# Optimization experiments

Hardware: AMD Instinct MI355X
Metric: run time of the kernel (lower is better)

Reference implementation:

```python
import jax, jax.numpy as jnp
import numpy as np

B, N, F, H, MH = 8, 1024, 768, 12, 3072
DH = F // H
EPS = 1e-5

def _ln(x, g, b):
    mu = jnp.mean(x, axis=-1, keepdims=True)
    var = jnp.mean(jnp.square(x - mu), axis=-1, keepdims=True)
    return (x - mu) * jax.lax.rsqrt(var + EPS) * g + b

def setup_inputs() -> dict:
    key = jax.random.key(0)
    ks = jax.random.split(key, 16)
    s = 1.0 / np.sqrt(F)
    sm = 1.0 / np.sqrt(MH)
    return {
        "x": jax.random.normal(ks[0], (B, N, F), dtype=jnp.float32),
        "Wq": jax.random.uniform(ks[1], (F, F), jnp.float32, -s, s),
        "bq": jax.random.uniform(ks[2], (F,), jnp.float32, -s, s),
        "Wk": jax.random.uniform(ks[3], (F, F), jnp.float32, -s, s),
        "bk": jax.random.uniform(ks[4], (F,), jnp.float32, -s, s),
        "Wv": jax.random.uniform(ks[5], (F, F), jnp.float32, -s, s),
        "bv": jax.random.uniform(ks[6], (F,), jnp.float32, -s, s),
        "Wo": jax.random.uniform(ks[7], (F, F), jnp.float32, -s, s),
        "bo": jax.random.uniform(ks[8], (F,), jnp.float32, -s, s),
        "ln1_g": jnp.ones((F,), jnp.float32),
        "ln1_b": jnp.zeros((F,), jnp.float32),
        "ln2_g": jnp.ones((F,), jnp.float32),
        "ln2_b": jnp.zeros((F,), jnp.float32),
        "W1": jax.random.uniform(ks[9], (F, MH), jnp.float32, -s, s),
        "b1": jax.random.uniform(ks[10], (MH,), jnp.float32, -s, s),
        "W2": jax.random.uniform(ks[11], (MH, F), jnp.float32, -sm, sm),
        "b2": jax.random.uniform(ks[12], (F,), jnp.float32, -sm, sm),
    }

def reference(x, Wq, bq, Wk, bk, Wv, bv, Wo, bo, ln1_g, ln1_b, ln2_g, ln2_b, W1, b1, W2, b2):
    xn = _ln(x, ln1_g, ln1_b)
    # low-rank (here full-rank, rank=-1) QKV projections, split into heads -> [b,h,n,dh]
    q = (xn @ Wq + bq).reshape(B, N, H, DH).transpose(0, 2, 1, 3)
    k = (xn @ Wk + bk).reshape(B, N, H, DH).transpose(0, 2, 1, 3)
    v = (xn @ Wv + bv).reshape(B, N, H, DH).transpose(0, 2, 1, 3)
    # note: original scales by sqrt(feats), NOT sqrt(d_head)
    score = jax.nn.softmax(jnp.einsum('bhif,bhjf->bhij', q, k) / jnp.sqrt(jnp.float32(F)), axis=-1)
    attn = jnp.einsum('bhij,bhjf->bhif', score, v)
    attn = attn.transpose(0, 2, 1, 3).reshape(B, N, F)
    out = (attn @ Wo + bo) + x  # dropout p=0.0
    h = _ln(out, ln2_g, ln2_b)
    h = jax.nn.gelu(h @ W1 + b1, approximate=False)
    h = jax.nn.gelu(h @ W2 + b2, approximate=False)  # second GELU per source
    return h + out
```

## Files before the change

kernel.cpp:

```cpp
#include <hip/hip_runtime.h>
#include <math.h>

#define B_ 8
#define N_ 1024
#define F_ 768
#define H_ 12
#define DH_ 64
#define MH_ 3072
#define MROWS (B_ * N_)

typedef unsigned short u16;
typedef unsigned int u32;
typedef __bf16 bf16x8 __attribute__((ext_vector_type(8)));
typedef float f32x4 __attribute__((ext_vector_type(4)));

__device__ inline f32x4 mfma16(bf16x8 a, bf16x8 b, f32x4 c) {
  return __builtin_amdgcn_mfma_f32_16x16x32_bf16(a, b, c, 0, 0, 0);
}

__device__ inline u16 f2bu(float f) {
  u32 b = __builtin_bit_cast(u32, f);
  b += 0x7fffu + ((b >> 16) & 1u);
  return (u16)(b >> 16);
}
__device__ inline float bu2f(u16 u) {
  u32 x = ((u32)u) << 16;
  return __builtin_bit_cast(float, x);
}
__device__ inline float gelu_f(float x) {
  float u = x * (0.7978845608028654f + 0.035677408136300125f * x * x);
  float t = exp2f(-2.8853900817779268f * fabsf(u));
  float th = (1.0f - t) / (1.0f + t);
  th = copysignf(th, u);
  return 0.5f * x * (1.0f + th);
}

#define AS1 __attribute__((address_space(1)))
#define AS3 __attribute__((address_space(3)))
__device__ inline void glds16(const void* g, void* l) {
  __builtin_amdgcn_global_load_lds((const AS1 void*)g, (AS3 void*)l, 16, 0, 0);
}

__global__ __launch_bounds__(256) void prep_weights(
    const float* __restrict__ Wq, const float* __restrict__ Wk,
    const float* __restrict__ Wv, const float* __restrict__ Wo,
    const float* __restrict__ W1, const float* __restrict__ W2,
    u16* __restrict__ Wqkvt, u16* __restrict__ Wot,
    u16* __restrict__ W1t, u16* __restrict__ W2t) {
  __shared__ float tile[64][65];
  int z = blockIdx.z;
  const float* in; u16* out; int R, C;
  if (z == 0)      { in = Wq; out = Wqkvt;                       R = 768;  C = 768; }
  else if (z == 1) { in = Wk; out = Wqkvt + 768 * 768;           R = 768;  C = 768; }
  else if (z == 2) { in = Wv; out = Wqkvt + 2 * 768 * 768;       R = 768;  C = 768; }
  else if (z == 3) { in = Wo; out = Wot;                         R = 768;  C = 768; }
  else if (z == 4) { in = W1; out = W1t;                         R = 768;  C = 3072; }
  else             { in = W2; out = W2t;                         R = 3072; C = 768; }
  int r0 = blockIdx.y << 6, c0 = blockIdx.x << 6;
  if (r0 >= R || c0 >= C) return;
  int t = threadIdx.x;
#pragma unroll
  for (int i = 0; i < 16; ++i) {
    int idx = t + (i << 8);
    int r = idx >> 6, c = idx & 63;
    tile[r][c] = in[(size_t)(r0 + r) * C + (c0 + c)];
  }
  __syncthreads();
#pragma unroll
  for (int i = 0; i < 16; ++i) {
    int idx = t + (i << 8);
    int rr = idx >> 6, cc = idx & 63;
    out[(size_t)(c0 + rr) * R + (r0 + cc)] = f2bu(tile[cc][rr]);
  }
}

__device__ inline float ldf(const float* p) { return *p; }
__device__ inline float ldf(const u16* p) { return bu2f(*p); }

template <typename Tin>
__global__ __launch_bounds__(256) void ln_to_bf16(
    const Tin* __restrict__ X, const float* __restrict__ gw,
    const float* __restrict__ bw, u16* __restrict__ Y) {
  int row = blockIdx.x;
  int t = threadIdx.x;
  const Tin* xr = X + (size_t)row * F_;
  float v0 = ldf(&xr[t]), v1 = ldf(&xr[t + 256]), v2 = ldf(&xr[t + 512]);
  float s = v0 + v1 + v2;
  float ss = v0 * v0 + v1 * v1 + v2 * v2;
#pragma unroll
  for (int off = 1; off < 64; off <<= 1) {
    s += __shfl_xor(s, off, 64);
    ss += __shfl_xor(ss, off, 64);
  }
  __shared__ float red[8];
  int wid = t >> 6, lane = t & 63;
  if (lane == 0) { red[wid] = s; red[4 + wid] = ss; }
  __syncthreads();
  s = red[0] + red[1] + red[2] + red[3];
  ss = red[4] + red[5] + red[6] + red[7];
  float mu = s * (1.0f / F_);
  float var = ss * (1.0f / F_) - mu * mu;
  float rstd = rsqrtf(var + 1e-5f);
  u16* yr = Y + (size_t)row * F_;
  yr[t] = f2bu((v0 - mu) * rstd * gw[t] + bw[t]);
  yr[t + 256] = f2bu((v1 - mu) * rstd * gw[t + 256] + bw[t + 256]);
  yr[t + 512] = f2bu((v2 - mu) * rstd * gw[t + 512] + bw[t + 512]);
}

template <int MODE>
__global__ __launch_bounds__(256, 2) void gemm_t(
    const u16* __restrict__ A, const u16* __restrict__ Bt,
    const float* __restrict__ b0, const float* __restrict__ b1,
    const float* __restrict__ b2, void* __restrict__ outp,
    const void* __restrict__ resid, int Ndim, int Kdim, float qscale) {
  __shared__ __attribute__((aligned(16))) u16 As[2][2][128][32];
  __shared__ __attribute__((aligned(16))) u16 Bs[2][2][128][32];
  int t = threadIdx.x;
  int lane = t & 63, wid = t >> 6;

  int nwg = gridDim.x;
  int q8 = nwg >> 3;
  int bid = blockIdx.x;
  int swz = (bid & 7) * q8 + (bid >> 3);
  int nnt = Ndim >> 7;
  int mt = swz / nnt, nt = swz - mt * nnt;
  int row0 = mt << 7, col0 = nt << 7;

  int wr = (wid >> 1) << 6;
  int wc = (wid & 1) << 6;
  int lr = lane & 15, lk = (lane >> 4) << 3;
  int rbase = (lane >> 4) << 2;
  f32x4 zero = {0.f, 0.f, 0.f, 0.f};
  f32x4 acc[4][4];
#pragma unroll
  for (int m = 0; m < 4; ++m)
#pragma unroll
    for (int n = 0; n < 4; ++n) acc[m][n] = zero;

  int srow = (wid << 5) + (lane >> 2);
  int scol = (lane & 3) << 3;
  const u16* Ag = A + (size_t)(row0 + srow) * Kdim + scol;
  const u16* Bg = Bt + (size_t)(col0 + srow) * Kdim + scol;
  char* AsB = (char*)&As[0][0][0][0] + (wid << 11);
  char* BsB = (char*)&Bs[0][0][0][0] + (wid << 11);

  auto STAGE = [&](int buf, int kt) {
    int ab = buf << 14;
#pragma unroll
    for (int kh = 0; kh < 2; ++kh) {
#pragma unroll
      for (int i = 0; i < 2; ++i) {
        glds16(Ag + (size_t)(i << 4) * Kdim + kt + (kh << 5),
               AsB + ab + (kh << 13) + (i << 10));
        glds16(Bg + (size_t)(i << 4) * Kdim + kt + (kh << 5),
               BsB + ab + (kh << 13) + (i << 10));
      }
    }
  };

  int nk = Kdim >> 6;
  STAGE(0, 0);
  if (nk > 1) STAGE(1, 64);

  for (int ki = 0; ki < nk; ++ki) {
    int buf = ki & 1;
    if (ki + 1 < nk) {
      asm volatile("s_waitcnt vmcnt(8)" ::: "memory");
    } else {
      asm volatile("s_waitcnt vmcnt(0)" ::: "memory");
    }
    __builtin_amdgcn_sched_barrier(0);
    __builtin_amdgcn_s_barrier();
    __builtin_amdgcn_sched_barrier(0);
    bf16x8 af[2][4], bfr[2][4];
#pragma unroll
    for (int h = 0; h < 2; ++h) {
#pragma unroll
      for (int m = 0; m < 4; ++m)
        af[h][m] = *(const bf16x8*)&As[buf][h][wr + (m << 4) + lr][lk];
#pragma unroll
      for (int n = 0; n < 4; ++n)
        bfr[h][n] = *(const bf16x8*)&Bs[buf][h][wc + (n << 4) + lr][lk];
    }
    __builtin_amdgcn_sched_barrier(0);
    __builtin_amdgcn_s_barrier();
    __builtin_amdgcn_sched_barrier(0);
    if (ki + 2 < nk) STAGE(buf, (ki + 2) << 6);
    __builtin_amdgcn_s_setprio(1);
#pragma unroll
    for (int h = 0; h < 2; ++h)
#pragma unroll
      for (int m = 0; m < 4; ++m)
#pragma unroll
        for (int n = 0; n < 4; ++n) acc[m][n] = mfma16(af[h][m], bfr[h][n], acc[m][n]);
    __builtin_amdgcn_s_setprio(0);
  }

#pragma unroll
  for (int n = 0; n < 4; ++n) {
    int col = col0 + wc + (n << 4) + lr;
    float bc;
    int sub = 0, hh = 0, dh = 0;
    float sc = 1.0f;
    if constexpr (MODE == 0) {
      sub = (col >= 1536) ? 2 : (col >= 768 ? 1 : 0);
      int c = col - sub * 768;
      bc = (sub == 0) ? b0[c] : (sub == 1 ? b1[c] : b2[c]);
      hh = c >> 6; dh = c & 63;
      sc = (sub == 0) ? qscale : 1.0f;
    } else {
      bc = b0[col];
    }
#pragma unroll
    for (int m = 0; m < 4; ++m) {
#pragma unroll
      for (int r = 0; r < 4; ++r) {
        int row = row0 + wr + (m << 4) + rbase + r;
        float val = acc[m][n][r] + bc;
        if constexpr (MODE == 0) {
          int bb = row >> 10, nn = row & 1023;
          if (sub < 2) {
            ((u16*)outp)[(size_t)sub * 6291456 +
                         ((((size_t)bb * H_ + hh) << 10) + nn) * DH_ + dh] = f2bu(val * sc);
          } else {
            ((u16*)outp)[(size_t)2 * 6291456 +
                         ((((size_t)bb * H_ + hh) << 6) + dh) * 1024 + nn] = f2bu(val);
          }
        } else {
          ((u16*)outp)[(size_t)row * Ndim + col] = f2bu(gelu_f(val));
        }
      }
    }
  }
}

template <int MODE>
__global__ __launch_bounds__(256, 3) void gemm_s(
    const u16* __restrict__ A, const u16* __restrict__ Bt,
    const float* __restrict__ bias, void* __restrict__ outp,
    const void* __restrict__ resid, int Ndim, int Kdim) {
  __shared__ __attribute__((aligned(16))) u16 As[2][2][128][32];
  __shared__ __attribute__((aligned(16))) u16 Bs[2][2][64][32];
  int t = threadIdx.x;
  int lane = t & 63, wid = t >> 6;

  int nwg = gridDim.x;
  int q8 = nwg >> 3;
  int bid = blockIdx.x;
  int swz = (bid & 7) * q8 + (bid >> 3);
  int nnt = Ndim >> 6;
  int mt = swz / nnt, nt = swz - mt * nnt;
  int row0 = mt << 7, col0 = nt << 6;

  int wr = (wid >> 1) << 6;
  int wc = (wid & 1) << 5;
  int lr = lane & 15, lk = (lane >> 4) << 3;
  int rbase = (lane >> 4) << 2;
  f32x4 zero = {0.f, 0.f, 0.f, 0.f};
  f32x4 acc[4][2];
#pragma unroll
  for (int m = 0; m < 4; ++m)
#pragma unroll
    for (int n = 0; n < 2; ++n) acc[m][n] = zero;

  int sarow = (wid << 5) + (lane >> 2);
  int sbrow = (wid << 4) + (lane >> 2);
  int scol = (lane & 3) << 3;
  const u16* Ag = A + (size_t)(row0 + sarow) * Kdim + scol;
  const u16* Bg = Bt + (size_t)(col0 + sbrow) * Kdim + scol;
  char* AsB = (char*)&As[0][0][0][0] + (wid << 11);
  char* BsB = (char*)&Bs[0][0][0][0] + (wid << 10);

  auto STAGE = [&](int buf, int kt) {
    int ab = buf << 14, bb = buf << 13;
#pragma unroll
    for (int kh = 0; kh < 2; ++kh) {
#pragma unroll
      for (int i = 0; i < 2; ++i)
        glds16(Ag + (size_t)(i << 4) * Kdim + kt + (kh << 5),
               AsB + ab + (kh << 13) + (i << 10));
      glds16(Bg + kt + (kh << 5), BsB + bb + (kh << 12));
    }
  };

  int nk = Kdim >> 6;
  STAGE(0, 0);
  if (nk > 1) STAGE(1, 64);

  for (int ki = 0; ki < nk; ++ki) {
    int buf = ki & 1;
    if (ki + 1 < nk) {
      asm volatile("s_waitcnt vmcnt(6)" ::: "memory");
    } else {
      asm volatile("s_waitcnt vmcnt(0)" ::: "memory");
    }
    __builtin_amdgcn_sched_barrier(0);
    __builtin_amdgcn_s_barrier();
    __builtin_amdgcn_sched_barrier(0);
    bf16x8 af[2][4], bfr[2][2];
#pragma unroll
    for (int h = 0; h < 2; ++h) {
#pragma unroll
      for (int m = 0; m < 4; ++m)
        af[h][m] = *(const bf16x8*)&As[buf][h][wr + (m << 4) + lr][lk];
#pragma unroll
      for (int n = 0; n < 2; ++n)
        bfr[h][n] = *(const bf16x8*)&Bs[buf][h][wc + (n << 4) + lr][lk];
    }
    __builtin_amdgcn_sched_barrier(0);
    __builtin_amdgcn_s_barrier();
    __builtin_amdgcn_sched_barrier(0);
    if (ki + 2 < nk) STAGE(buf, (ki + 2) << 6);
    __builtin_amdgcn_s_setprio(1);
#pragma unroll
    for (int h = 0; h < 2; ++h)
#pragma unroll
      for (int m = 0; m < 4; ++m)
#pragma unroll
        for (int n = 0; n < 2; ++n) acc[m][n] = mfma16(af[h][m], bfr[h][n], acc[m][n]);
    __builtin_amdgcn_s_setprio(0);
  }

#pragma unroll
  for (int n = 0; n < 2; ++n) {
    int col = col0 + wc + (n << 4) + lr;
    float bc = bias[col];
#pragma unroll
    for (int m = 0; m < 4; ++m) {
#pragma unroll
      for (int r = 0; r < 4; ++r) {
        int row = row0 + wr + (m << 4) + rbase + r;
        float val = acc[m][n][r] + bc;
        if constexpr (MODE == 1) {
          val += ((const float*)resid)[(size_t)row * Ndim + col];
          ((u16*)outp)[(size_t)row * Ndim + col] = f2bu(val);
        } else {
          val = gelu_f(val) + bu2f(((const u16*)resid)[(size_t)row * Ndim + col]);
          ((float*)outp)[(size_t)row * Ndim + col] = val;
        }
      }
    }
  }
}

__global__ __launch_bounds__(256, 3) void attn_fwd(
    const u16* __restrict__ Q, const u16* __restrict__ K,
    const u16* __restrict__ Vt, u16* __restrict__ Aout) {
  __shared__ __attribute__((aligned(16))) u16 Ks[64][72];
  __shared__ __attribute__((aligned(16))) u16 Vs[64][72];
  __shared__ __attribute__((aligned(16))) u16 Ps[4][32][72];
  int t = threadIdx.x, lane = t & 63, wid = t >> 6;

  int bid = blockIdx.x;
  int swz = (bid & 7) * 96 + (bid >> 3);
  int bh = swz >> 3;
  int qt = swz & 7;
  int q0 = (qt << 7) + (wid << 5);

  int lr = lane & 15, lk = (lane >> 4) << 3;
  int rbase = (lane >> 4) << 2;

  bf16x8 qf[2][2];
#pragma unroll
  for (int m = 0; m < 2; ++m)
#pragma unroll
    for (int ks = 0; ks < 2; ++ks)
      qf[m][ks] = *(const bf16x8*)&Q[((size_t)bh * N_ + q0 + (m << 4) + lr) * DH_ + (ks << 5) + lk];

  float lsum[2][4];
  f32x4 zero = {0.f, 0.f, 0.f, 0.f};
  f32x4 Oacc[2][4];
#pragma unroll
  for (int m = 0; m < 2; ++m) {
#pragma unroll
    for (int r = 0; r < 4; ++r) lsum[m][r] = 0.f;
#pragma unroll
    for (int nd = 0; nd < 4; ++nd) Oacc[m][nd] = zero;
  }

  int srow = t >> 3;
  int scol = (t & 7) << 3;
  const u16* Kg = K + ((size_t)bh * N_ + srow) * DH_ + scol;
  const u16* Vg = Vt + ((size_t)bh * DH_ + srow) * N_ + scol;

  uint4 kr0, kr1, vr0, vr1;
  auto LOADKV = [&](int kt) {
    kr0 = *(const uint4*)(Kg + (size_t)(kt << 6) * DH_);
    kr1 = *(const uint4*)(Kg + (size_t)((kt << 6) + 32) * DH_);
    vr0 = *(const uint4*)(Vg + (kt << 6));
    vr1 = *(const uint4*)(Vg + (size_t)32 * N_ + (kt << 6));
  };
  LOADKV(0);

  for (int kt = 0; kt < 16; ++kt) {
    __syncthreads();
    *(uint4*)&Ks[srow][scol]      = kr0;
    *(uint4*)&Ks[srow + 32][scol] = kr1;
    *(uint4*)&Vs[srow][scol]      = vr0;
    *(uint4*)&Vs[srow + 32][scol] = vr1;
    if (kt + 1 < 16) LOADKV(kt + 1);
    __syncthreads();

    f32x4 s[2][4];
#pragma unroll
    for (int m = 0; m < 2; ++m)
#pragma unroll
      for (int n = 0; n < 4; ++n) s[m][n] = zero;
#pragma unroll
    for (int ks = 0; ks < 2; ++ks) {
      bf16x8 kf[4];
#pragma unroll
      for (int n = 0; n < 4; ++n) kf[n] = *(const bf16x8*)&Ks[(n << 4) + lr][(ks << 5) + lk];
#pragma unroll
      for (int m = 0; m < 2; ++m)
#pragma unroll
        for (int n = 0; n < 4; ++n) s[m][n] = mfma16(qf[m][ks], kf[n], s[m][n]);
    }

#pragma unroll
    for (int m = 0; m < 2; ++m)
#pragma unroll
      for (int n = 0; n < 4; ++n)
#pragma unroll
        for (int r = 0; r < 4; ++r) {
          float p = exp2f(s[m][n][r]);
          lsum[m][r] += p;
          Ps[wid][(m << 4) + rbase + r][(n << 4) + lr] = f2bu(p);
        }

#pragma unroll
    for (int ks = 0; ks < 2; ++ks) {
      bf16x8 pf[2], vf[4];
#pragma unroll
      for (int m = 0; m < 2; ++m) pf[m] = *(const bf16x8*)&Ps[wid][(m << 4) + lr][(ks << 5) + lk];
#pragma unroll
      for (int nd = 0; nd < 4; ++nd) vf[nd] = *(const bf16x8*)&Vs[(nd << 4) + lr][(ks << 5) + lk];
#pragma unroll
      for (int m = 0; m < 2; ++m)
#pragma unroll
        for (int nd = 0; nd < 4; ++nd) Oacc[m][nd] = mfma16(pf[m], vf[nd], Oacc[m][nd]);
    }
  }

  int b = bh / H_, h = bh % H_;
#pragma unroll
  for (int m = 0; m < 2; ++m)
#pragma unroll
    for (int r = 0; r < 4; ++r) {
      float sv = lsum[m][r];
#pragma unroll
      for (int off = 1; off < 16; off <<= 1) sv += __shfl_xor(sv, off, 64);
      float inv = 1.0f / sv;
      int row = q0 + (m << 4) + rbase + r;
      size_t orow = ((size_t)b * N_ + row) * F_ + (size_t)h * DH_;
#pragma unroll
      for (int nd = 0; nd < 4; ++nd)
        Aout[orow + (nd << 4) + lr] = f2bu(Oacc[m][nd][r] * inv);
    }
}

extern "C" void kernel_launch(void* const* d_in, const int* in_sizes, int n_in,
                              void* d_out, int out_size, void* d_ws, size_t ws_size,
                              hipStream_t stream) {
  (void)in_sizes; (void)n_in; (void)out_size; (void)ws_size;
  const float* x   = (const float*)d_in[0];
  const float* Wq  = (const float*)d_in[1];
  const float* bq  = (const float*)d_in[2];
  const float* Wk  = (const float*)d_in[3];
  const float* bk  = (const float*)d_in[4];
  const float* Wv  = (const float*)d_in[5];
  const float* bv  = (const float*)d_in[6];
  const float* Wo  = (const float*)d_in[7];
  const float* bo  = (const float*)d_in[8];
  const float* g1  = (const float*)d_in[9];
  const float* bn1 = (const float*)d_in[10];
  const float* g2  = (const float*)d_in[11];
  const float* bn2 = (const float*)d_in[12];
  const float* W1  = (const float*)d_in[13];
  const float* b1  = (const float*)d_in[14];
  const float* W2  = (const float*)d_in[15];
  const float* b2  = (const float*)d_in[16];

  char* ws = (char*)d_ws;
  size_t off = 0;
  auto alloc = [&](size_t bytes) {
    char* p = ws + off;
    off += (bytes + 255) & ~(size_t)255;
    return p;
  };
  u16* Wqkvt = (u16*)alloc((size_t)3 * F_ * F_ * 2);
  u16* Wot  = (u16*)alloc((size_t)F_ * F_ * 2);
  u16* W1t  = (u16*)alloc((size_t)MH_ * F_ * 2);
  u16* W2t  = (u16*)alloc((size_t)MH_ * F_ * 2);
  u16* xn  = (u16*)alloc((size_t)MROWS * F_ * 2);
  u16* qb  = (u16*)alloc((size_t)B_ * H_ * N_ * DH_ * 2);
  u16* kb  = (u16*)alloc((size_t)B_ * H_ * N_ * DH_ * 2);
  u16* vt  = (u16*)alloc((size_t)B_ * H_ * N_ * DH_ * 2);
  u16* pad = (u16*)alloc((size_t)B_ * H_ * N_ * DH_ * 2);
  u16* attn = (u16*)alloc((size_t)MROWS * F_ * 2);
  u16* outb = (u16*)alloc((size_t)MROWS * F_ * 2);
  u16* h1 = qb;
  u16* hn = xn;
  (void)pad;

  const float QSCALE = 0.052058773227f;

  dim3 blk(256);
  prep_weights<<<dim3(48, 48, 6), blk, 0, stream>>>(Wq, Wk, Wv, Wo, W1, W2,
                                                    Wqkvt, Wot, W1t, W2t);
  ln_to_bf16<float><<<dim3(MROWS), blk, 0, stream>>>(x, g1, bn1, xn);
  gemm_t<0><<<dim3(64 * 18), blk, 0, stream>>>(xn, Wqkvt, bq, bk, bv, qb,
                                               nullptr, 3 * F_, F_, QSCALE);
  attn_fwd<<<dim3(768), blk, 0, stream>>>(qb, kb, vt, attn);
  gemm_s<1><<<dim3(64 * 12), blk, 0, stream>>>(attn, Wot, bo, outb, x, F_, F_);
  ln_to_bf16<u16><<<dim3(MROWS), blk, 0, stream>>>(outb, g2, bn2, hn);
  gemm_t<2><<<dim3(64 * 24), blk, 0, stream>>>(hn, W1t, b1, nullptr, nullptr,
                                               h1, nullptr, MH_, F_, 1.0f);
  gemm_s<3><<<dim3(64 * 12), blk, 0, stream>>>(h1, W2t, b2, d_out, outb, F_, MH_);
}
```

Baseline: 277.9 us.

## Compact weight-prep grid, separate V transpose, retile output and MLP2 GEMMs

Several changes land together. The weight-prep launch becomes a flat grid with no idle blocks. The QKV GEMM now writes V in row layout, and a new transpose kernel builds V^T, which makes the scattered per-element V stores contiguous. The attention-output projection moves to gemm_t with a residual-add mode. The MLP2 GEMM is retiled from 128x64 to 64x128 tiles. The extra transpose kernel adds a launch plus another pass over V, and gemm_t<1> on a 384-block grid may underfill the device.

```diff
diff --git a/kernel.cpp b/kernel.cpp
--- a/kernel.cpp
+++ b/kernel.cpp
@@ -48,16 +48,19 @@
     u16* __restrict__ Wqkvt, u16* __restrict__ Wot,
     u16* __restrict__ W1t, u16* __restrict__ W2t) {
   __shared__ float tile[64][65];
-  int z = blockIdx.z;
+  int id = blockIdx.x;
+  int z, bx, by;
+  if (id < 576) { z = id / 144; int l = id % 144; bx = l % 12; by = l / 12; }
+  else if (id < 1152) { z = 4; int l = id - 576; bx = l % 48; by = l / 48; }
+  else { z = 5; int l = id - 1152; bx = l % 12; by = l / 12; }
   const float* in; u16* out; int R, C;
-  if (z == 0)      { in = Wq; out = Wqkvt;                       R = 768;  C = 768; }
-  else if (z == 1) { in = Wk; out = Wqkvt + 768 * 768;           R = 768;  C = 768; }
-  else if (z == 2) { in = Wv; out = Wqkvt + 2 * 768 * 768;       R = 768;  C = 768; }
-  else if (z == 3) { in = Wo; out = Wot;                         R = 768;  C = 768; }
-  else if (z == 4) { in = W1; out = W1t;                         R = 768;  C = 3072; }
-  else             { in = W2; out = W2t;                         R = 3072; C = 768; }
-  int r0 = blockIdx.y << 6, c0 = blockIdx.x << 6;
-  if (r0 >= R || c0 >= C) return;
+  if (z == 0)      { in = Wq; out = Wqkvt;                 R = 768;  C = 768; }
+  else if (z == 1) { in = Wk; out = Wqkvt + 768 * 768;     R = 768;  C = 768; }
+  else if (z == 2) { in = Wv; out = Wqkvt + 2 * 768 * 768; R = 768;  C = 768; }
+  else if (z == 3) { in = Wo; out = Wot;                   R = 768;  C = 768; }
+  else if (z == 4) { in = W1; out = W1t;                   R = 768;  C = 3072; }
+  else             { in = W2; out = W2t;                   R = 3072; C = 768; }
+  int r0 = by << 6, c0 = bx << 6;
   int t = threadIdx.x;
 #pragma unroll
   for (int i = 0; i < 16; ++i) {
@@ -71,6 +74,27 @@
     int idx = t + (i << 8);
     int rr = idx >> 6, cc = idx & 63;
     out[(size_t)(c0 + rr) * R + (r0 + cc)] = f2bu(tile[cc][rr]);
+  }
+}
+
+__global__ __launch_bounds__(256) void transpose_v(
+    const u16* __restrict__ in, u16* __restrict__ out, int R, int C) {
+  __shared__ float tile[64][65];
+  size_t base = (size_t)blockIdx.z * (size_t)R * (size_t)C;
+  int r0 = blockIdx.y << 6, c0 = blockIdx.x << 6;
+  int t = threadIdx.x;
+#pragma unroll
+  for (int i = 0; i < 16; ++i) {
+    int idx = t + (i << 8);
+    int r = idx >> 6, c = idx & 63;
+    tile[r][c] = bu2f(in[base + (size_t)(r0 + r) * C + (c0 + c)]);
+  }
+  __syncthreads();
+#pragma unroll
+  for (int i = 0; i < 16; ++i) {
+    int idx = t + (i << 8);
+    int rr = idx >> 6, cc = idx & 63;
+    out[base + (size_t)(c0 + rr) * R + (r0 + cc)] = f2bu(tile[cc][rr]);
   }
 }
 
@@ -219,13 +243,11 @@
         float val = acc[m][n][r] + bc;
         if constexpr (MODE == 0) {
           int bb = row >> 10, nn = row & 1023;
-          if (sub < 2) {
-            ((u16*)outp)[(size_t)sub * 6291456 +
-                         ((((size_t)bb * H_ + hh) << 10) + nn) * DH_ + dh] = f2bu(val * sc);
-          } else {
-            ((u16*)outp)[(size_t)2 * 6291456 +
-                         ((((size_t)bb * H_ + hh) << 6) + dh) * 1024 + nn] = f2bu(val);
-          }
+          ((u16*)outp)[(size_t)sub * 6291456 +
+                       ((((size_t)bb * H_ + hh) << 10) + nn) * DH_ + dh] = f2bu(val * sc);
+        } else if constexpr (MODE == 1) {
+          val += ((const float*)resid)[(size_t)row * Ndim + col];
+          ((u16*)outp)[(size_t)row * Ndim + col] = f2bu(val);
         } else {
           ((u16*)outp)[(size_t)row * Ndim + col] = f2bu(gelu_f(val));
         }
@@ -234,13 +256,12 @@
   }
 }
 
-template <int MODE>
-__global__ __launch_bounds__(256, 3) void gemm_s(
+__global__ __launch_bounds__(256, 3) void gemm_w(
     const u16* __restrict__ A, const u16* __restrict__ Bt,
     const float* __restrict__ bias, void* __restrict__ outp,
-    const void* __restrict__ resid, int Ndim, int Kdim) {
-  __shared__ __attribute__((aligned(16))) u16 As[2][2][128][32];
-  __shared__ __attribute__((aligned(16))) u16 Bs[2][2][64][32];
+    const u16* __restrict__ resid, int Ndim, int Kdim) {
+  __shared__ __attribute__((aligned(16))) u16 As[2][2][64][32];
+  __shared__ __attribute__((aligned(16))) u16 Bs[2][2][128][32];
   int t = threadIdx.x;
   int lane = t & 63, wid = t >> 6;
 
@@ -248,38 +269,39 @@
   int q8 = nwg >> 3;
   int bid = blockIdx.x;
   int swz = (bid & 7) * q8 + (bid >> 3);
-  int nnt = Ndim >> 6;
+  int nnt = Ndim >> 7;
   int mt = swz / nnt, nt = swz - mt * nnt;
-  int row0 = mt << 7, col0 = nt << 6;
-
-  int wr = (wid >> 1) << 6;
-  int wc = (wid & 1) << 5;
+  int row0 = mt << 6, col0 = nt << 7;
+
+  int wr = (wid >> 1) << 5;
+  int wc = (wid & 1) << 6;
   int lr = lane & 15, lk = (lane >> 4) << 3;
   int rbase = (lane >> 4) << 2;
   f32x4 zero = {0.f, 0.f, 0.f, 0.f};
-  f32x4 acc[4][2];
-#pragma unroll
-  for (int m = 0; m < 4; ++m)
-#pragma unroll
-    for (int n = 0; n < 2; ++n) acc[m][n] = zero;
-
-  int sarow = (wid << 5) + (lane >> 2);
-  int sbrow = (wid << 4) + (lane >> 2);
+  f32x4 acc[2][4];
+#pragma unroll
+  for (int m = 0; m < 2; ++m)
+#pragma unroll
+    for (int n = 0; n < 4; ++n) acc[m][n] = zero;
+
+  int sarow = (wid << 4) + (lane >> 2);
+  int sbrow = (wid << 5) + (lane >> 2);
   int scol = (lane & 3) << 3;
   const u16* Ag = A + (size_t)(row0 + sarow) * Kdim + scol;
   const u16* Bg = Bt + (size_t)(col0 + sbrow) * Kdim + scol;
-  char* AsB = (char*)&As[0][0][0][0] + (wid << 11);
-  char* BsB = (char*)&Bs[0][0][0][0] + (wid << 10);
+  char* AsB = (char*)&As[0][0][0][0] + (wid << 10);
+  char* BsB = (char*)&Bs[0][0][0][0] + (wid << 11);
 
   auto STAGE = [&](int buf, int kt) {
-    int ab = buf << 14, bb = buf << 13;
+    int ab = buf << 13;
+    int bb = buf << 14;
 #pragma unroll
     for (int kh = 0; kh < 2; ++kh) {
+      glds16(Ag + kt + (kh << 5), AsB + ab + (kh << 12));
 #pragma unroll
       for (int i = 0; i < 2; ++i)
-        glds16(Ag + (size_t)(i << 4) * Kdim + kt + (kh << 5),
-               AsB + ab + (kh << 13) + (i << 10));
-      glds16(Bg + kt + (kh << 5), BsB + bb + (kh << 12));
+        glds16(Bg + (size_t)(i << 4) * Kdim + kt + (kh << 5),
+               BsB + bb + (kh << 13) + (i << 10));
     }
   };
 
@@ -297,14 +319,14 @@
     __builtin_amdgcn_sched_barrier(0);
     __builtin_amdgcn_s_barrier();
     __builtin_amdgcn_sched_barrier(0);
-    bf16x8 af[2][4], bfr[2][2];
+    bf16x8 af[2][2], bfr[2][4];
 #pragma unroll
     for (int h = 0; h < 2; ++h) {
 #pragma unroll
-      for (int m = 0; m < 4; ++m)
+      for (int m = 0; m < 2; ++m)
         af[h][m] = *(const bf16x8*)&As[buf][h][wr + (m << 4) + lr][lk];
 #pragma unroll
-      for (int n = 0; n < 2; ++n)
+      for (int n = 0; n < 4; ++n)
         bfr[h][n] = *(const bf16x8*)&Bs[buf][h][wc + (n << 4) + lr][lk];
     }
     __builtin_amdgcn_sched_barrier(0);
@@ -315,29 +337,24 @@
 #pragma unroll
     for (int h = 0; h < 2; ++h)
 #pragma unroll
-      for (int m = 0; m < 4; ++m)
-#pragma unroll
-        for (int n = 0; n < 2; ++n) acc[m][n] = mfma16(af[h][m], bfr[h][n], acc[m][n]);
+      for (int m = 0; m < 2; ++m)
+#pragma unroll
+        for (int n = 0; n < 4; ++n) acc[m][n] = mfma16(af[h][m], bfr[h][n], acc[m][n]);
     __builtin_amdgcn_s_setprio(0);
   }
 
 #pragma unroll
-  for (int n = 0; n < 2; ++n) {
+  for (int n = 0; n < 4; ++n) {
     int col = col0 + wc + (n << 4) + lr;
     float bc = bias[col];
 #pragma unroll
-    for (int m = 0; m < 4; ++m) {
+    for (int m = 0; m < 2; ++m) {
 #pragma unroll
       for (int r = 0; r < 4; ++r) {
         int row = row0 + wr + (m << 4) + rbase + r;
         float val = acc[m][n][r] + bc;
-        if constexpr (MODE == 1) {
-          val += ((const float*)resid)[(size_t)row * Ndim + col];
-          ((u16*)outp)[(size_t)row * Ndim + col] = f2bu(val);
-        } else {
-          val = gelu_f(val) + bu2f(((const u16*)resid)[(size_t)row * Ndim + col]);
-          ((float*)outp)[(size_t)row * Ndim + col] = val;
-        }
+        val = gelu_f(val) + bu2f(resid[(size_t)row * Ndim + col]);
+        ((float*)outp)[(size_t)row * Ndim + col] = val;
       }
     }
   }
@@ -495,26 +512,28 @@
   u16* xn  = (u16*)alloc((size_t)MROWS * F_ * 2);
   u16* qb  = (u16*)alloc((size_t)B_ * H_ * N_ * DH_ * 2);
   u16* kb  = (u16*)alloc((size_t)B_ * H_ * N_ * DH_ * 2);
+  u16* vb  = (u16*)alloc((size_t)B_ * H_ * N_ * DH_ * 2);
   u16* vt  = (u16*)alloc((size_t)B_ * H_ * N_ * DH_ * 2);
-  u16* pad = (u16*)alloc((size_t)B_ * H_ * N_ * DH_ * 2);
   u16* attn = (u16*)alloc((size_t)MROWS * F_ * 2);
   u16* outb = (u16*)alloc((size_t)MROWS * F_ * 2);
   u16* h1 = qb;
   u16* hn = xn;
-  (void)pad;
+  (void)vb;
 
   const float QSCALE = 0.052058773227f;
 
   dim3 blk(256);
-  prep_weights<<<dim3(48, 48, 6), blk, 0, stream>>>(Wq, Wk, Wv, Wo, W1, W2,
-                                                    Wqkvt, Wot, W1t, W2t);
+  prep_weights<<<dim3(1728), blk, 0, stream>>>(Wq, Wk, Wv, Wo, W1, W2,
+                                               Wqkvt, Wot, W1t, W2t);
   ln_to_bf16<float><<<dim3(MROWS), blk, 0, stream>>>(x, g1, bn1, xn);
   gemm_t<0><<<dim3(64 * 18), blk, 0, stream>>>(xn, Wqkvt, bq, bk, bv, qb,
                                                nullptr, 3 * F_, F_, QSCALE);
+  transpose_v<<<dim3(1, 16, 96), blk, 0, stream>>>(vb, vt, N_, DH_);
   attn_fwd<<<dim3(768), blk, 0, stream>>>(qb, kb, vt, attn);
-  gemm_s<1><<<dim3(64 * 12), blk, 0, stream>>>(attn, Wot, bo, outb, x, F_, F_);
+  gemm_t<1><<<dim3(64 * 6), blk, 0, stream>>>(attn, Wot, bo, nullptr, nullptr,
+                                              outb, x, F_, F_, 1.0f);
   ln_to_bf16<u16><<<dim3(MROWS), blk, 0, stream>>>(outb, g2, bn2, hn);
   gemm_t<2><<<dim3(64 * 24), blk, 0, stream>>>(hn, W1t, b1, nullptr, nullptr,
                                                h1, nullptr, MH_, F_, 1.0f);
-  gemm_s<3><<<dim3(64 * 12), blk, 0, stream>>>(h1, W2t, b2, d_out, outb, F_, MH_);
-}
+  gemm_w<<<dim3(128 * 6), blk, 0, stream>>>(h1, W2t, b2, d_out, outb, F_, MH_);
+}
```

New measurement: 266.1 us. 1.04x faster.
